# Performance work log

Hardware: AMD Instinct MI355X
Metric: run time of the kernel (lower is better)

## Reference

```python
import jax, jax.numpy as jnp
import numpy as np

B, S, D, H = 4, 2048, 512, 8
E = D // H  # d_head = 64

def setup_inputs() -> dict:
    key = jax.random.key(0)
    ks = jax.random.split(key, 10)
    s_in = (1.0 / np.sqrt(D))
    x  = jax.random.normal(ks[0], (B, S, D), dtype=jnp.float32)
    Wq = jax.random.normal(ks[1], (H, D, E), dtype=jnp.float32) * s_in
    bq = jax.random.normal(ks[2], (H, E), dtype=jnp.float32) * 0.01
    Wk = jax.random.normal(ks[3], (H, D, E), dtype=jnp.float32) * s_in
    bk = jax.random.normal(ks[4], (H, E), dtype=jnp.float32) * 0.01
    Wv = jax.random.normal(ks[5], (H, D, E), dtype=jnp.float32) * s_in
    bv = jax.random.normal(ks[6], (H, E), dtype=jnp.float32) * 0.01
    Wo = jax.random.normal(ks[7], (D, D), dtype=jnp.float32) * s_in
    bo = jax.random.normal(ks[8], (D,), dtype=jnp.float32) * 0.01
    return {"x": x, "Wq": Wq, "bq": bq, "Wk": Wk, "bk": bk,
            "Wv": Wv, "bv": bv, "Wo": Wo, "bo": bo}

def reference(x, Wq, bq, Wk, bk, Wv, bv, Wo, bo):
    B_, S_, D_ = x.shape
    # per-head projections (batched over head axis h)
    q = jnp.einsum('bsd,hde->bhse', x, Wq) + bq[None, :, None, :]
    k = jnp.einsum('bsd,hde->bhse', x, Wk) + bk[None, :, None, :]
    v = jnp.einsum('bsd,hde->bhse', x, Wv) + bv[None, :, None, :]
    # NOTE: original scales by d_model**-0.5 (full D), not d_head**-0.5
    scale = jnp.asarray(D_, x.dtype) ** -0.5
    scores = jnp.einsum('bhse,bhte->bhst', q, k) * scale  # [B,H,S,S]
    causal = jnp.tril(jnp.ones((S_, S_), dtype=bool))
    scores = jnp.where(causal[None, None], scores, -jnp.inf)
    attn = jax.nn.softmax(scores, axis=-1)
    out = jnp.einsum('bhst,bhte->bhse', attn, v)  # [B,H,S,E]
    # concat heads along feature dim (head-major), matching torch.cat
    out = out.transpose(0, 2, 1, 3).reshape(B_, S_, D_)
    return out @ Wo + bo  # final projection; dropout never applied in source
```

## Files before the change

### kernel.cpp

```cpp
#include <hip/hip_runtime.h>

typedef unsigned short u16;
typedef __bf16 bf16x8 __attribute__((ext_vector_type(8)));
typedef short s16x4 __attribute__((ext_vector_type(4)));
typedef short s16x8 __attribute__((ext_vector_type(8)));
typedef float f32x4 __attribute__((ext_vector_type(4)));

#define BB 4
#define SS 2048
#define DD 512
#define HH 8
#define EE 64
#define MM 8192
#define BHSE (BB*HH*SS*EE)

#define GLOBAL_AS __attribute__((address_space(1)))
#define LDS_AS    __attribute__((address_space(3)))

__device__ __forceinline__ float b2f(u16 u) {
    return __uint_as_float(((unsigned int)u) << 16);
}
__device__ __forceinline__ u16 f2b(float f) {
    unsigned int v = __float_as_uint(f);
    v += 0x7fffu + ((v >> 16) & 1u);
    return (u16)(v >> 16);
}
__device__ __forceinline__ float loadE(const void* p, size_t idx, int isbf16) {
    return isbf16 ? b2f(((const u16*)p)[idx]) : ((const float*)p)[idx];
}
__device__ __forceinline__ f32x4 mfma16x16x16_bf16(s16x4 a, s16x4 b, f32x4 c) {
    return __builtin_amdgcn_mfma_f32_16x16x16bf16_1k(a, b, c, 0, 0, 0);
}
__device__ __forceinline__ void load_lds16(const u16* g, u16* l) {
    __builtin_amdgcn_global_load_lds((GLOBAL_AS void*)g, (LDS_AS void*)l, 16, 0, 0);
}

__device__ __forceinline__ int detect_bf16_wave(const u16* x) {
    const int lane = threadIdx.x & 63;
    float a0 = fabsf(b2f(x[2 * lane]));
    float a1 = fabsf(b2f(x[2 * (lane + 64)]));
    int c0 = (a0 == 0.f) || (a0 > 1e-4f && a0 < 100.f);
    int c1 = (a1 == 0.f) || (a1 > 1e-4f && a1 < 100.f);
    int cnt = __popcll(__ballot(c0)) + __popcll(__ballot(c1));
    return cnt >= 96;
}

__global__ __launch_bounds__(256) void prep(
    const void* __restrict__ X,
    const void* __restrict__ Wq, const void* __restrict__ Wk,
    const void* __restrict__ Wv, const void* __restrict__ Wo,
    u16* __restrict__ Xb, u16* __restrict__ WT, u16* __restrict__ WoT,
    int* __restrict__ flag)
{
    const int isbf16 = detect_bf16_wave((const u16*)X);
    const int bid = blockIdx.x;
    const int tid = threadIdx.x;
    if (bid < 1024) {
        if (bid == 0 && tid == 0) *flag = isbf16;
        const size_t i0 = ((size_t)bid * 256 + tid) * 16;
        if (isbf16) {
            const uint4* src = (const uint4*)(((const u16*)X) + i0);
            uint4* dst = (uint4*)(Xb + i0);
            dst[0] = src[0];
            dst[1] = src[1];
        } else {
            const float* xf = ((const float*)X) + i0;
            float4 f0 = *(const float4*)xf;
            float4 f1 = *(const float4*)(xf + 4);
            float4 f2 = *(const float4*)(xf + 8);
            float4 f3 = *(const float4*)(xf + 12);
            u16 tmp[16] = { f2b(f0.x), f2b(f0.y), f2b(f0.z), f2b(f0.w),
                            f2b(f1.x), f2b(f1.y), f2b(f1.z), f2b(f1.w),
                            f2b(f2.x), f2b(f2.y), f2b(f2.z), f2b(f2.w),
                            f2b(f3.x), f2b(f3.y), f2b(f3.z), f2b(f3.w) };
            *(uint4*)(Xb + i0) = *(const uint4*)tmp;
            *(uint4*)(Xb + i0 + 8) = *(const uint4*)(tmp + 8);
        }
        return;
    }
    const int j = bid - 1024;
    const int job = j >> 6;
    const int t = j & 63;
    const void* src; u16* dst; int src_ld;
    if (job < 3) {
        const void* W = (job == 0) ? Wq : ((job == 1) ? Wk : Wv);
        int h = t >> 3, kt = t & 7;
        size_t off = (size_t)h * DD * EE + (size_t)kt * 64 * EE;
        src = isbf16 ? (const void*)(((const u16*)W) + off)
                     : (const void*)(((const float*)W) + off);
        src_ld = EE;
        dst = WT + (size_t)job * 512 * 512 + (size_t)(h * 64) * 512 + kt * 64;
    } else {
        int a = t >> 3, b = t & 7;
        size_t off = (size_t)(a * 64) * 512 + b * 64;
        src = isbf16 ? (const void*)(((const u16*)Wo) + off)
                     : (const void*)(((const float*)Wo) + off);
        src_ld = 512;
        dst = WoT + (size_t)(b * 64) * 512 + a * 64;
    }
    __shared__ __align__(16) u16 Ts[64 * 72];
#pragma unroll
    for (int it = 0; it < 2; ++it) {
        int idx = it * 256 + tid;
        int r = idx >> 3, c = (idx & 7) << 3;
        u16 tmp[8];
        if (isbf16) {
            *(bf16x8*)tmp = *(const bf16x8*)(((const u16*)src) + (size_t)r * src_ld + c);
        } else {
            const float* sp = ((const float*)src) + (size_t)r * src_ld + c;
            float4 f0 = *(const float4*)sp;
            float4 f1 = *(const float4*)(sp + 4);
            tmp[0] = f2b(f0.x); tmp[1] = f2b(f0.y); tmp[2] = f2b(f0.z); tmp[3] = f2b(f0.w);
            tmp[4] = f2b(f1.x); tmp[5] = f2b(f1.y); tmp[6] = f2b(f1.z); tmp[7] = f2b(f1.w);
        }
#pragma unroll
        for (int k = 0; k < 8; ++k) Ts[(c + k) * 72 + r] = tmp[k];
    }
    __syncthreads();
#pragma unroll
    for (int it = 0; it < 2; ++it) {
        int idx = it * 256 + tid;
        int r = idx >> 3, c = (idx & 7) << 3;
        *(bf16x8*)(dst + (size_t)r * 512 + c) = *(const bf16x8*)&Ts[r * 72 + c];
    }
}

template<int MT, int NT>
__device__ __forceinline__ void mfma_step(const u16* As, const u16* Bs,
    int mh, int nh, int lq, int quad, f32x4 acc[MT][NT])
{
    const int sw = lq & 7;
#pragma unroll
    for (int kw = 0; kw < 2; ++kw) {
        const int G = kw * 4 + quad;
        const int col = ((G ^ sw) << 3);
        bf16x8 a[MT], b[NT];
#pragma unroll
        for (int mt = 0; mt < MT; ++mt)
            a[mt] = *(const bf16x8*)&As[(mh + mt * 16 + lq) * 64 + col];
#pragma unroll
        for (int nt = 0; nt < NT; ++nt)
            b[nt] = *(const bf16x8*)&Bs[(nh + nt * 16 + lq) * 64 + col];
#pragma unroll
        for (int mt = 0; mt < MT; ++mt)
#pragma unroll
            for (int nt = 0; nt < NT; ++nt)
                acc[mt][nt] = __builtin_amdgcn_mfma_f32_16x16x32_bf16(a[mt], b[nt], acc[mt][nt], 0, 0, 0);
    }
}

__global__ __launch_bounds__(256) void gemm_qkv(
    const u16* __restrict__ Xb, const u16* __restrict__ WT,
    const void* __restrict__ bq, const void* __restrict__ bk,
    const void* __restrict__ bv, u16* __restrict__ qkv,
    const int* __restrict__ flag)
{
    const float SCALE = 0.04419417382415922f;
    const int isbf16 = *flag;
    const int l = blockIdx.x;
    const int m0 = ((l & 7) * 8 + ((l >> 3) & 7)) * 128;
    const int n0 = (l >> 6) * 128;
    const int tid = threadIdx.x;
    const int wave = tid >> 6, lane = tid & 63;
    const int lq = lane & 15, quad = lane >> 4;
    const int mh = (wave & 1) * 64, nh = (wave >> 1) * 64;
    __shared__ __align__(16) u16 As[128 * 64];
    __shared__ __align__(16) u16 Bs[128 * 64];
    f32x4 acc[4][4] = {};

    const int swz = (lane & 7) ^ ((lane >> 3) & 7);
    const size_t lane_off = (size_t)(lane >> 3) * 512 + 8 * swz;

    for (int k0 = 0; k0 < 512; k0 += 64) {
        __syncthreads();
#pragma unroll
        for (int jj = 0; jj < 4; ++jj) {
            const int c = wave * 4 + jj;
            load_lds16(Xb + (size_t)(m0 + 8 * c) * 512 + k0 + lane_off, &As[c * 512]);
            load_lds16(WT + (size_t)(n0 + 8 * c) * 512 + k0 + lane_off, &Bs[c * 512]);
        }
        __syncthreads();
        mfma_step<4, 4>(As, Bs, mh, nh, lq, quad, acc);
    }

    const int proj = n0 >> 9;
    const void* bias = (proj == 0) ? bq : ((proj == 1) ? bk : bv);
#pragma unroll
    for (int mt = 0; mt < 4; ++mt) {
#pragma unroll
        for (int nt = 0; nt < 4; ++nt) {
#pragma unroll
            for (int r = 0; r < 4; ++r) {
                int m = m0 + mh + mt * 16 + quad * 4 + r;
                int n = n0 + nh + nt * 16 + lq;
                int nn = n & 511;
                float v = acc[mt][nt][r] + loadE(bias, nn, isbf16);
                if (proj == 0) v *= SCALE;
                int b_ = m >> 11, s = m & 2047, h = nn >> 6, e = nn & 63;
                qkv[(size_t)proj * BHSE + (((size_t)(b_ * HH + h) * SS + s) * EE + e)] = f2b(v);
            }
        }
    }
}

struct Stage { uint4 k0, k1, va, vb; };

__device__ __forceinline__ void stage_load(Stage& st, const u16* Kh, const u16* Vh,
                                           int t0, int tid) {
    int r = tid >> 3, c = (tid & 7) * 8;
    st.k0 = *(const uint4*)(Kh + (size_t)(t0 + r) * 64 + c);
    st.k1 = *(const uint4*)(Kh + (size_t)(t0 + r + 32) * 64 + c);
    int t2 = 2 * (tid & 31), e8 = (tid >> 5) * 8;
    st.va = *(const uint4*)(Vh + (size_t)(t0 + t2) * 64 + e8);
    st.vb = *(const uint4*)(Vh + (size_t)(t0 + t2 + 1) * 64 + e8);
}
__device__ __forceinline__ void stage_write(const Stage& st, u16* Ksb, u16* VTsb, int tid) {
    int r = tid >> 3, c = (tid & 7) * 8;
    *(uint4*)(Ksb + r * 72 + c) = st.k0;
    *(uint4*)(Ksb + (r + 32) * 72 + c) = st.k1;
    int t2 = 2 * (tid & 31), e8 = (tid >> 5) * 8;
    int g2 = ((t2 >> 2) & 3) * 16 + ((t2 >> 4) << 2) + (t2 & 3);
    const unsigned* pa = (const unsigned*)&st.va;
    const unsigned* pb = (const unsigned*)&st.vb;
#pragma unroll
    for (int k = 0; k < 4; ++k) {
        unsigned lo = __builtin_amdgcn_perm(pb[k], pa[k], 0x05040100u);
        unsigned hi = __builtin_amdgcn_perm(pb[k], pa[k], 0x07060302u);
        *(unsigned*)(VTsb + (e8 + 2 * k) * 72 + g2) = lo;
        *(unsigned*)(VTsb + (e8 + 2 * k + 1) * 72 + g2) = hi;
    }
}

__device__ __forceinline__ void attn_tile(const u16* Ksb, const u16* VTsb,
    bf16x8 qf0, bf16x8 qf1, int lq, int quad, int wave, bool diag,
    f32x4 Ot[4], f32x4& lfrag)
{
    const s16x4 ones = { (short)0x3F80, (short)0x3F80, (short)0x3F80, (short)0x3F80 };
#pragma unroll
    for (int half = 0; half < 2; ++half) {
        s16x4 vf[4][2];
#pragma unroll
        for (int et = 0; et < 4; ++et) {
            const u16* Vp = VTsb + (et * 16 + lq) * 72 + quad * 16 + half * 8;
            s16x8 v = *(const s16x8*)Vp;
            vf[et][0] = __builtin_shufflevector(v, v, 0, 1, 2, 3);
            vf[et][1] = __builtin_shufflevector(v, v, 4, 5, 6, 7);
        }
#pragma unroll
        for (int tj = 0; tj < 2; ++tj) {
            const int tt = half * 2 + tj;
            const u16* Krow = Ksb + (tt * 16 + lq) * 72;
            bf16x8 k0 = *(const bf16x8*)(Krow + quad * 8);
            bf16x8 k1 = *(const bf16x8*)(Krow + 32 + quad * 8);
            f32x4 sc = {};
            sc = __builtin_amdgcn_mfma_f32_16x16x32_bf16(k0, qf0, sc, 0, 0, 0);
            sc = __builtin_amdgcn_mfma_f32_16x16x32_bf16(k1, qf1, sc, 0, 0, 0);
            unsigned pu[4];
#pragma unroll
            for (int r = 0; r < 4; ++r) {
                float p = __expf(sc[r]);
                if (diag) {
                    int tl = tt * 16 + quad * 4 + r;
                    int ql = 16 * wave + lq;
                    p = (tl <= ql) ? p : 0.f;
                }
                pu[r] = __float_as_uint(p);
            }
            union { unsigned u[2]; s16x4 s; } pf;
            pf.u[0] = __builtin_amdgcn_perm(pu[1], pu[0], 0x07060302u);
            pf.u[1] = __builtin_amdgcn_perm(pu[3], pu[2], 0x07060302u);
            lfrag = mfma16x16x16_bf16(ones, pf.s, lfrag);
#pragma unroll
            for (int et = 0; et < 4; ++et)
                Ot[et] = mfma16x16x16_bf16(vf[et][tj], pf.s, Ot[et]);
        }
    }
}

__global__ __launch_bounds__(256) void attn_kernel(
    const u16* __restrict__ Qg, const u16* __restrict__ Kg,
    const u16* __restrict__ Vg, u16* __restrict__ Og)
{
    const int bh = blockIdx.x;
    const int qb = ((int)gridDim.y - 1 - (int)blockIdx.y) * 64;
    const int nt = qb >> 6;
    const int tid = threadIdx.x;
    const int wave = tid >> 6, lane = tid & 63;
    const int lq = lane & 15, quad = lane >> 4;
    const int b = bh >> 3, h = bh & 7;

    const size_t base = (size_t)bh * SS * EE;
    const u16* Kh = Kg + base;
    const u16* Vh = Vg + base;

    __shared__ __align__(16) u16 Ks[2][64 * 72];
    __shared__ __align__(16) u16 VTs[2][64 * 72];

    const int qrow = qb + 16 * wave + lq;
    const u16* Qp = Qg + base + (size_t)qrow * EE;
    bf16x8 qf0 = *(const bf16x8*)(Qp + quad * 8);
    bf16x8 qf1 = *(const bf16x8*)(Qp + 32 + quad * 8);

    f32x4 Ot[4] = {};
    f32x4 lfrag = {};

    Stage st;
    stage_load(st, Kh, Vh, 0, tid);
    stage_write(st, Ks[0], VTs[0], tid);
    for (int i = 0; i <= nt; ++i) {
        __syncthreads();
        const int cur = i & 1;
        const bool more = (i < nt);
        if (more) stage_load(st, Kh, Vh, (i + 1) * 64, tid);
        attn_tile(Ks[cur], VTs[cur], qf0, qf1, lq, quad, wave, i == nt, Ot, lfrag);
        if (more) stage_write(st, Ks[cur ^ 1], VTs[cur ^ 1], tid);
    }

    const float inv = 1.f / lfrag[0];

    u16* Op = Og + (((size_t)(b * SS + qrow)) * HH + h) * EE;
#pragma unroll
    for (int et = 0; et < 4; ++et) {
        u16 tmp[4];
#pragma unroll
        for (int r = 0; r < 4; ++r) tmp[r] = f2b(Ot[et][r] * inv);
        *(uint2*)(Op + et * 16 + quad * 4) = *(const uint2*)tmp;
    }
}

__global__ __launch_bounds__(256) void gemm_out(
    const u16* __restrict__ A, const u16* __restrict__ WoT,
    const void* __restrict__ bo, void* __restrict__ out,
    const int* __restrict__ flag)
{
    const int isbf16 = *flag;
    const int l = blockIdx.x;
    const int m0 = ((l & 7) * 8 + ((l >> 3) & 7)) * 128;
    const int n0 = (l >> 6) * 64;
    const int tid = threadIdx.x;
    const int wave = tid >> 6, lane = tid & 63;
    const int lq = lane & 15, quad = lane >> 4;
    const int mh = (wave & 1) * 64, nh = (wave >> 1) * 32;
    __shared__ __align__(16) u16 As[128 * 64];
    __shared__ __align__(16) u16 Bs[64 * 64];
    f32x4 acc[4][2] = {};

    const int swz = (lane & 7) ^ ((lane >> 3) & 7);
    const size_t lane_off = (size_t)(lane >> 3) * 512 + 8 * swz;

    for (int k0 = 0; k0 < 512; k0 += 64) {
        __syncthreads();
#pragma unroll
        for (int jj = 0; jj < 4; ++jj) {
            const int c = wave * 4 + jj;
            load_lds16(A + (size_t)(m0 + 8 * c) * 512 + k0 + lane_off, &As[c * 512]);
        }
#pragma unroll
        for (int jj = 0; jj < 2; ++jj) {
            const int c = wave * 2 + jj;
            load_lds16(WoT + (size_t)(n0 + 8 * c) * 512 + k0 + lane_off, &Bs[c * 512]);
        }
        __syncthreads();
        mfma_step<4, 2>(As, Bs, mh, nh, lq, quad, acc);
    }
#pragma unroll
    for (int mt = 0; mt < 4; ++mt) {
#pragma unroll
        for (int nt = 0; nt < 2; ++nt) {
#pragma unroll
            for (int r = 0; r < 4; ++r) {
                int m = m0 + mh + mt * 16 + quad * 4 + r;
                int n = n0 + nh + nt * 16 + lq;
                float v = acc[mt][nt][r] + loadE(bo, n, isbf16);
                if (isbf16) ((u16*)out)[(size_t)m * 512 + n] = f2b(v);
                else        ((float*)out)[(size_t)m * 512 + n] = v;
            }
        }
    }
}

extern "C" void kernel_launch(void* const* d_in, const int* in_sizes, int n_in,
                              void* d_out, int out_size, void* d_ws, size_t ws_size,
                              hipStream_t stream) {
    const void* x  = d_in[0];
    const void* Wq = d_in[1];
    const void* bq = d_in[2];
    const void* Wk = d_in[3];
    const void* bk = d_in[4];
    const void* Wv = d_in[5];
    const void* bv = d_in[6];
    const void* Wo = d_in[7];
    const void* bo = d_in[8];

    u16* WT   = (u16*)d_ws;
    u16* WoT  = WT + 3 * 512 * 512;
    u16* qkv  = WoT + 512 * 512;
    u16* attn = qkv + 3 * (size_t)BHSE;
    int* flag = (int*)(attn + (size_t)BHSE);
    u16* Xb   = (u16*)(flag + 8);

    prep<<<1024 + 256, 256, 0, stream>>>(x, Wq, Wk, Wv, Wo, Xb, WT, WoT, flag);
    gemm_qkv<<<(MM / 128) * (1536 / 128), 256, 0, stream>>>(Xb, WT, bq, bk, bv, qkv, flag);
    attn_kernel<<<dim3(BB * HH, SS / 64), 256, 0, stream>>>(qkv, qkv + BHSE, qkv + 2 * (size_t)BHSE, attn);
    gemm_out<<<(MM / 128) * (512 / 64), 256, 0, stream>>>(attn, WoT, bo, d_out, flag);
}
```

Measured before the change: 189.0 us.

## Split long causal attention rows across two KV chunks with a merge kernel

Query blocks in the second half of the sequence now have their KV range split into two chunks of up to 16 tiles, run as separate blocks on a third grid dimension. Each chunk writes unnormalized fp32 partial outputs and row sums to workspace, and a new merge kernel adds the partials and normalizes. The aim is to shorten the longest blocks and balance the causal workload, at the cost of extra fp32 traffic, an additional launch and empty early-exit blocks. Merging without max rescaling is valid only because the tile routine appears to work without a running max.

```diff
diff --git a/kernel.cpp b/kernel.cpp
--- a/kernel.cpp
+++ b/kernel.cpp
@@ -279,11 +279,20 @@
 
 __global__ __launch_bounds__(256) void attn_kernel(
     const u16* __restrict__ Qg, const u16* __restrict__ Kg,
-    const u16* __restrict__ Vg, u16* __restrict__ Og)
+    const u16* __restrict__ Vg, u16* __restrict__ Og,
+    float* __restrict__ Opart, float* __restrict__ Lpart)
 {
     const int bh = blockIdx.x;
-    const int qb = ((int)gridDim.y - 1 - (int)blockIdx.y) * 64;
-    const int nt = qb >> 6;
+    const int j  = (int)gridDim.y - 1 - (int)blockIdx.y;
+    const int c  = blockIdx.z;
+    if (c && j < 16) return;
+    const int qb = j * 64;
+    const int tFirst = c * 16;
+    const int tLast  = (j < tFirst + 15) ? j : (tFirst + 15);
+    const int nIt = tLast - tFirst;
+    const bool diagHere = (tLast == j);
+    const bool partial = (j >= 16);
+
     const int tid = threadIdx.x;
     const int wave = tid >> 6, lane = tid & 63;
     const int lq = lane & 15, quad = lane >> 4;
@@ -305,27 +314,71 @@
     f32x4 lfrag = {};
 
     Stage st;
-    stage_load(st, Kh, Vh, 0, tid);
+    stage_load(st, Kh, Vh, tFirst * 64, tid);
     stage_write(st, Ks[0], VTs[0], tid);
-    for (int i = 0; i <= nt; ++i) {
+    for (int i = 0; i <= nIt; ++i) {
         __syncthreads();
         const int cur = i & 1;
-        const bool more = (i < nt);
-        if (more) stage_load(st, Kh, Vh, (i + 1) * 64, tid);
-        attn_tile(Ks[cur], VTs[cur], qf0, qf1, lq, quad, wave, i == nt, Ot, lfrag);
+        const bool more = (i < nIt);
+        if (more) stage_load(st, Kh, Vh, (tFirst + i + 1) * 64, tid);
+        attn_tile(Ks[cur], VTs[cur], qf0, qf1, lq, quad, wave,
+                  diagHere && (i == nIt), Ot, lfrag);
         if (more) stage_write(st, Ks[cur ^ 1], VTs[cur ^ 1], tid);
     }
 
-    const float inv = 1.f / lfrag[0];
-
-    u16* Op = Og + (((size_t)(b * SS + qrow)) * HH + h) * EE;
-#pragma unroll
-    for (int et = 0; et < 4; ++et) {
-        u16 tmp[4];
-#pragma unroll
-        for (int r = 0; r < 4; ++r) tmp[r] = f2b(Ot[et][r] * inv);
-        *(uint2*)(Op + et * 16 + quad * 4) = *(const uint2*)tmp;
-    }
+    if (!partial) {
+        const float inv = 1.f / lfrag[0];
+        u16* Op = Og + (((size_t)(b * SS + qrow)) * HH + h) * EE;
+#pragma unroll
+        for (int et = 0; et < 4; ++et) {
+            u16 tmp[4];
+#pragma unroll
+            for (int r = 0; r < 4; ++r) tmp[r] = f2b(Ot[et][r] * inv);
+            *(uint2*)(Op + et * 16 + quad * 4) = *(const uint2*)tmp;
+        }
+    } else {
+        const size_t slot = ((size_t)(bh * 16 + (j - 16)) * 2 + c);
+        float* Os = Opart + slot * 4096;
+        const int ql = 16 * wave + lq;
+#pragma unroll
+        for (int et = 0; et < 4; ++et)
+            *(f32x4*)&Os[ql * 64 + et * 16 + quad * 4] = Ot[et];
+        if (quad == 0) Lpart[slot * 64 + ql] = lfrag[0];
+    }
+}
+
+__global__ __launch_bounds__(256) void attn_merge(
+    const float* __restrict__ Opart, const float* __restrict__ Lpart,
+    u16* __restrict__ Og)
+{
+    const int tg = blockIdx.x * 256 + threadIdx.x;
+    const int e8 = (tg & 7) * 8;
+    const int rest = tg >> 3;
+    const int bh = rest >> 10;
+    const int sp = rest & 1023;
+    const int jj = sp >> 6;
+    const int ql = sp & 63;
+    const size_t slot = (size_t)(bh * 16 + jj) * 2;
+    const size_t o0 = slot * 4096 + (size_t)ql * 64 + e8;
+    float4 a0 = *(const float4*)&Opart[o0];
+    float4 a1 = *(const float4*)&Opart[o0 + 4];
+    float4 b0 = *(const float4*)&Opart[o0 + 4096];
+    float4 b1 = *(const float4*)&Opart[o0 + 4096 + 4];
+    const size_t ls = slot * 64 + ql;
+    const float inv = 1.f / (Lpart[ls] + Lpart[ls + 64]);
+    const int b = bh >> 3, h = bh & 7;
+    const int s = 1024 + sp;
+    u16 tmp[8];
+    tmp[0] = f2b((a0.x + b0.x) * inv);
+    tmp[1] = f2b((a0.y + b0.y) * inv);
+    tmp[2] = f2b((a0.z + b0.z) * inv);
+    tmp[3] = f2b((a0.w + b0.w) * inv);
+    tmp[4] = f2b((a1.x + b1.x) * inv);
+    tmp[5] = f2b((a1.y + b1.y) * inv);
+    tmp[6] = f2b((a1.z + b1.z) * inv);
+    tmp[7] = f2b((a1.w + b1.w) * inv);
+    u16* Op = Og + (((size_t)(b * SS + s)) * HH + h) * EE + e8;
+    *(uint4*)Op = *(const uint4*)tmp;
 }
 
 __global__ __launch_bounds__(256) void gemm_out(
@@ -398,9 +451,13 @@
     u16* attn = qkv + 3 * (size_t)BHSE;
     int* flag = (int*)(attn + (size_t)BHSE);
     u16* Xb   = (u16*)(flag + 8);
+    float* Opart = (float*)(Xb + (size_t)MM * DD);
+    float* Lpart = Opart + (size_t)1024 * 4096;
 
     prep<<<1024 + 256, 256, 0, stream>>>(x, Wq, Wk, Wv, Wo, Xb, WT, WoT, flag);
     gemm_qkv<<<(MM / 128) * (1536 / 128), 256, 0, stream>>>(Xb, WT, bq, bk, bv, qkv, flag);
-    attn_kernel<<<dim3(BB * HH, SS / 64), 256, 0, stream>>>(qkv, qkv + BHSE, qkv + 2 * (size_t)BHSE, attn);
+    attn_kernel<<<dim3(BB * HH, SS / 64, 2), 256, 0, stream>>>(
+        qkv, qkv + BHSE, qkv + 2 * (size_t)BHSE, attn, Opart, Lpart);
+    attn_merge<<<1024, 256, 0, stream>>>(Opart, Lpart, attn);
     gemm_out<<<(MM / 128) * (512 / 64), 256, 0, stream>>>(attn, WoT, bo, d_out, flag);
 }
```

Result: faster. 184.3 us (-2.5%).
